# Performance work log

Measured on AMD Instinct MI355X. Metric: run time of the kernel, lower is better.

Reference implementation:

```python
import jax, jax.numpy as jnp
import numpy as np

ROUTINGS = 3
NUM_CAPSULE = 32
DIM_CAPSULE = 64
K_EPSILON = 1e-7  # keras K.epsilon()


def squash(x, axis=-1):
    s = jnp.sum(jnp.square(x), axis=axis, keepdims=True) + K_EPSILON
    scale = jnp.sqrt(s) / (0.5 + s)
    return scale * x


def setup_inputs() -> dict:
    key = jax.random.key(0)
    k1, k2 = jax.random.split(key)
    B, N_in, D_in = 32, 1024, 512
    u = jax.random.normal(k1, (B, N_in, D_in), dtype=jnp.float32)
    # glorot_uniform for capsule_kernel (conv1d width-1 kernel == dense matrix)
    fan_out = NUM_CAPSULE * DIM_CAPSULE
    limit = float(np.sqrt(6.0 / (D_in + fan_out)))
    W = jax.random.uniform(k2, (D_in, fan_out), jnp.float32, -limit, limit)
    return {"u": u, "W": W}


def reference(u, W):
    B, N_in, _ = u.shape
    # K.conv1d with width-1 kernel == matmul, then reshape
    u_hat = (u @ W).reshape(B, N_in, NUM_CAPSULE, DIM_CAPSULE)
    u_hat = jnp.transpose(u_hat, (0, 2, 1, 3))  # [B, N_out, N_in, D]
    b = jnp.zeros(u_hat.shape[:3], u_hat.dtype)  # [B, N_out, N_in]
    vj = None
    for i in range(ROUTINGS):
        Wv = jax.nn.softmax(b, axis=1)  # softmax over output capsules (axis=1)
        vj = jnp.einsum('bon,bond->bod', Wv, u_hat)  # batch_dot(Wv,u_hat,[2,2])
        if i < ROUTINGS - 1:
            # K.l2_normalize(vj) with default axis=None -> global L2 norm
            norm = jnp.sqrt(jnp.maximum(jnp.sum(jnp.square(vj)), 1e-12))
            vjn = vj / norm
            b = jnp.einsum('bod,bond->bon', vjn, u_hat)  # batch_dot(vj,u_hat,[2,3])
    return squash(vj)
```

## Files before the change

kernel.cpp:

```cpp
#include <hip/hip_runtime.h>
#include <hip/hip_bf16.h>


constexpr int B = 32, N = 1024, K = 512, O = 32, D = 64, F = 2048;
constexpr int NT = 32;
constexpr int ST = 72;
constexpr int STW = 40;

typedef __attribute__((ext_vector_type(8))) short bf16x8;
typedef __attribute__((ext_vector_type(4))) float f32x4;

__device__ inline unsigned int pk_hi(float x, float y) {
  union { __hip_bfloat162 h; unsigned int u; } c;
  c.h = __float22bfloat162_rn(float2{x, y});
  return c.u;
}
__device__ inline unsigned short bf16_1(float x) {
  return (unsigned short)(pk_hi(x, 0.f) & 0xffffu);
}
__device__ inline void split2(float x, unsigned short& h, unsigned short& l) {
  h = bf16_1(x);
  l = bf16_1(x - __uint_as_float((unsigned int)h << 16));
}
__device__ inline float bf2f(unsigned short h) {
  return __uint_as_float((unsigned int)h << 16);
}
__device__ inline int swz(int r) { return ((r >> 3) & 7) << 3; }

__device__ inline bf16x8 frag_row(const unsigned short* p, int r, int k0) {
  return *(const bf16x8*)&p[r * ST + (k0 ^ swz(r))];
}
__device__ inline bf16x8 frag_col(const unsigned short* p, int c, int n0) {
  bf16x8 f;
#pragma unroll
  for (int j = 0; j < 8; j++) {
    int n = n0 + j;
    f[j] = (short)p[n * ST + (c ^ swz(n))];
  }
  return f;
}

__global__ __launch_bounds__(256) void k_prep(const float* __restrict__ u,
                                              float* __restrict__ cs_part,
                                              unsigned short* __restrict__ u_bf) {
  __shared__ float4 red[128];
  int b = blockIdx.x, ntile = blockIdx.y, n0 = ntile * 32;
  int tid = threadIdx.x;
  int kq = (tid & 127) * 4, ng = tid >> 7;
  const float* ub = u + ((size_t)b * N + n0 + ng * 16) * K + kq;
  unsigned short* ubf = u_bf + ((size_t)b * N + n0 + ng * 16) * K + kq;
  float4 a = {0.f, 0.f, 0.f, 0.f};
#pragma unroll
  for (int nn = 0; nn < 16; nn++) {
    float4 v = *(const float4*)&ub[(size_t)nn * K];
    a.x += v.x; a.y += v.y; a.z += v.z; a.w += v.w;
    uint2 p;
    p.x = pk_hi(v.x, v.y);
    p.y = pk_hi(v.z, v.w);
    *(uint2*)&ubf[(size_t)nn * K] = p;
  }
  if (ng) red[tid & 127] = a;
  __syncthreads();
  if (!ng) {
    float4 o = red[tid];
    float* cs = cs_part + ((size_t)b * 32 + ntile) * K + kq;
    cs[0] = (a.x + o.x) * (1.f / 32.f);
    cs[1] = (a.y + o.y) * (1.f / 32.f);
    cs[2] = (a.z + o.z) * (1.f / 32.f);
    cs[3] = (a.w + o.w) * (1.f / 32.f);
  }
}

__global__ __launch_bounds__(512) void k_vjt(const unsigned short* __restrict__ Sp,
                                             const float* __restrict__ cs_part,
                                             const float* __restrict__ W,
                                             float* __restrict__ ssq_part, int slot,
                                             unsigned short* __restrict__ t_hi,
                                             unsigned short* __restrict__ t_lo) {
  __shared__ __align__(16) float s_s[K];
  __shared__ float red[7][D];
  __shared__ __align__(16) float vs[D];
  int bo = blockIdx.x, b = bo >> 5, o = bo & 31;
  int d = threadIdx.x & 63, ks = threadIdx.x >> 6;
  {
    int i = threadIdx.x;
    float a = 0.f;
    if (slot == 0) {
      const float* base = cs_part + (size_t)b * 32 * K;
#pragma unroll
      for (int nt = 0; nt < 32; nt++) a += base[(size_t)nt * K + i];
    } else {
      const unsigned short* base = Sp + ((size_t)b * NT * O + o) * K;
#pragma unroll
      for (int nt = 0; nt < NT; nt++) a += bf2f(base[(size_t)nt * O * K + i]);
    }
    s_s[i] = a;
  }
  __syncthreads();
  float acc = 0.f;
  const float* Wc = W + (size_t)o * D + d;
  for (int k = ks * 64; k < ks * 64 + 64; k += 4) {
    acc += s_s[k] * Wc[(size_t)k * F] + s_s[k + 1] * Wc[(size_t)(k + 1) * F] +
           s_s[k + 2] * Wc[(size_t)(k + 2) * F] + s_s[k + 3] * Wc[(size_t)(k + 3) * F];
  }
  if (ks) red[ks - 1][d] = acc;
  __syncthreads();
  if (ks == 0) {
#pragma unroll
    for (int j = 0; j < 7; j++) acc += red[j][d];
    vs[d] = acc;
    float ss = acc * acc;
#pragma unroll
    for (int m = 32; m >= 1; m >>= 1) ss += __shfl_xor(ss, m, 64);
    if (d == 0) ssq_part[slot * 1024 + bo] = ss;
  }
  __syncthreads();
  {
    int wave = threadIdx.x >> 6, lane = threadIdx.x & 63;
    int rr = lane >> 3, dc = lane & 7;
    float4 va = *(const float4*)&vs[dc * 8];
    float4 vb = *(const float4*)&vs[dc * 8 + 4];
#pragma unroll
    for (int i = 0; i < 8; i++) {
      int kk = wave * 64 + i * 8 + rr;
      const float* Wr = W + (size_t)kk * F + o * 64 + dc * 8;
      float4 wa = *(const float4*)Wr;
      float4 wb = *(const float4*)(Wr + 4);
      float p = wa.x * va.x + wa.y * va.y + wa.z * va.z + wa.w * va.w +
                wb.x * vb.x + wb.y * vb.y + wb.z * vb.z + wb.w * vb.w;
      p += __shfl_xor(p, 1, 64);
      p += __shfl_xor(p, 2, 64);
      p += __shfl_xor(p, 4, 64);
      if (dc == 0) {
        unsigned short h, l;
        split2(p, h, l);
        t_hi[(size_t)bo * K + kk] = h;
        t_lo[(size_t)bo * K + kk] = l;
      }
    }
  }
}

__global__ __launch_bounds__(512) void k_out(const unsigned short* __restrict__ Sp,
                                             const float* __restrict__ W,
                                             float* __restrict__ out) {
  __shared__ __align__(16) float s_s[K];
  __shared__ float red[7][D];
  int bo = blockIdx.x, b = bo >> 5, o = bo & 31;
  int d = threadIdx.x & 63, ks = threadIdx.x >> 6;
  {
    const unsigned short* base = Sp + ((size_t)b * NT * O + o) * K;
    int i = threadIdx.x;
    float a = 0.f;
#pragma unroll
    for (int nt = 0; nt < NT; nt++) a += bf2f(base[(size_t)nt * O * K + i]);
    s_s[i] = a;
  }
  __syncthreads();
  float acc = 0.f;
  const float* Wc = W + (size_t)o * D + d;
  for (int k = ks * 64; k < ks * 64 + 64; k += 4) {
    acc += s_s[k] * Wc[(size_t)k * F] + s_s[k + 1] * Wc[(size_t)(k + 1) * F] +
           s_s[k + 2] * Wc[(size_t)(k + 2) * F] + s_s[k + 3] * Wc[(size_t)(k + 3) * F];
  }
  if (ks) red[ks - 1][d] = acc;
  __syncthreads();
  if (ks == 0) {
#pragma unroll
    for (int j = 0; j < 7; j++) acc += red[j][d];
    float ss = acc * acc;
#pragma unroll
    for (int m = 32; m >= 1; m >>= 1) ss += __shfl_xor(ss, m, 64);
    float s = ss + 1e-7f;
    out[(size_t)bo * D + d] = (sqrtf(s) / (0.5f + s)) * acc;
  }
}

__global__ __launch_bounds__(256, 2) void k_route(const unsigned short* __restrict__ t_hi_g,
                                                  const unsigned short* __restrict__ t_lo_g,
                                                  const unsigned short* __restrict__ u_bf,
                                                  const float* __restrict__ ssq_part,
                                                  int slot,
                                                  unsigned short* __restrict__ Sp) {
  __shared__ unsigned short u_res[8][32 * ST];
  __shared__ float wv[32 * 36];
  __shared__ float psum[8 * 36];
  __shared__ float mbuf[36];
  __shared__ unsigned short wvh[32 * STW], wvl[32 * STW];

  const int b = blockIdx.x;
  const int tid = threadIdx.x, lane = tid & 63, wave = tid >> 6;
  const int m = lane & 15, oct = lane >> 4;
  const unsigned short* thg = t_hi_g + (size_t)b * O * K;
  const unsigned short* tlg = t_lo_g + (size_t)b * O * K;

  const int sr = tid >> 3, sc8 = (tid & 7) * 8;
  const int scs = sc8 ^ swz(sr);

  float nrm_inv;
  {
    const float* sp = ssq_part + slot * 1024;
    float sa = 0.f;
#pragma unroll
    for (int j = 0; j < 4; j++) sa += sp[tid + j * 256];
    psum[tid] = sa;
    __syncthreads();
    if (tid < 64) {
      float s = psum[tid] + psum[tid + 64] + psum[tid + 128] + psum[tid + 192];
#pragma unroll
      for (int mm = 32; mm >= 1; mm >>= 1) s += __shfl_xor(s, mm, 64);
      if (tid == 0) mbuf[0] = rsqrtf(fmaxf(s, 1e-12f));
    }
    __syncthreads();
    nrm_inv = mbuf[0];
  }

  const int mo = wave & 1, nt = wave >> 1;
  const int mo2 = wave & 1, kp = wave >> 1;
  const int o0 = mo2 * 16;

  for (int ti = 0; ti < 2; ti++) {
    const int tile = blockIdx.y * 2 + ti;
    const unsigned short* ubf = u_bf + ((size_t)b * N + tile * 32) * K;

    __syncthreads();
#pragma unroll
    for (int ch = 0; ch < 8; ch++) {
      *(uint4*)&u_res[ch][sr * ST + scs] =
          *(const uint4*)&ubf[(size_t)sr * K + ch * 64 + sc8];
    }
    __syncthreads();

    f32x4 accb = {0.f, 0.f, 0.f, 0.f};
    for (int kcb = 0; kcb < 8; kcb++) {
      const unsigned short* uc = u_res[kcb];
      const size_t tb = (size_t)(mo * 16 + m) * K + kcb * 64;
#pragma unroll
      for (int ks = 0; ks < 64; ks += 32) {
        bf16x8 ah = *(const bf16x8*)&thg[tb + ks + oct * 8];
        bf16x8 al = *(const bf16x8*)&tlg[tb + ks + oct * 8];
        bf16x8 bh = frag_row(uc, nt * 16 + m, ks + oct * 8);
        accb = __builtin_amdgcn_mfma_f32_16x16x32_bf16(ah, bh, accb, 0, 0, 0);
        accb = __builtin_amdgcn_mfma_f32_16x16x32_bf16(al, bh, accb, 0, 0, 0);
      }
    }
#pragma unroll
    for (int r = 0; r < 4; r++)
      wv[(mo * 16 + oct * 4 + r) * 36 + nt * 16 + m] = accb[r] * nrm_inv;
    __syncthreads();

    {
      int n = tid & 31, g = tid >> 5;
      float m4 = -1e30f;
#pragma unroll
      for (int j = 0; j < 4; j++) m4 = fmaxf(m4, wv[(g * 4 + j) * 36 + n]);
      psum[g * 36 + n] = m4;
      __syncthreads();
      if (tid < 32) {
        float mx = psum[tid];
#pragma unroll
        for (int gg = 1; gg < 8; gg++) mx = fmaxf(mx, psum[gg * 36 + tid]);
        mbuf[tid] = mx;
      }
      __syncthreads();
      float mx = mbuf[n];
      float s4 = 0.f;
#pragma unroll
      for (int j = 0; j < 4; j++) {
        float e = __expf(wv[(g * 4 + j) * 36 + n] - mx);
        wv[(g * 4 + j) * 36 + n] = e;
        s4 += e;
      }
      psum[g * 36 + n] = s4;
      __syncthreads();
      if (tid < 32) {
        float s = 0.f;
#pragma unroll
        for (int gg = 0; gg < 8; gg++) s += psum[gg * 36 + tid];
        mbuf[tid] = 1.f / s;
      }
      __syncthreads();
      float inv = mbuf[n];
#pragma unroll
      for (int j = 0; j < 4; j++) {
        unsigned short h, l;
        split2(wv[(g * 4 + j) * 36 + n] * inv, h, l);
        wvh[(g * 4 + j) * STW + n] = h;
        wvl[(g * 4 + j) * STW + n] = l;
      }
    }
    __syncthreads();

    bf16x8 a_h = *(const bf16x8*)&wvh[(o0 + m) * STW + oct * 8];
    bf16x8 a_l = *(const bf16x8*)&wvl[(o0 + m) * STW + oct * 8];
    unsigned short* Sb = Sp + ((size_t)b * NT + tile) * O * K;
    for (int kcb = 0; kcb < 8; kcb++) {
      const unsigned short* uc = u_res[kcb];
#pragma unroll
      for (int kt = kp * 2; kt < kp * 2 + 2; kt++) {
        int c = kt * 16 + m;
        bf16x8 bh = frag_col(uc, c, oct * 8);
        f32x4 acs = {0.f, 0.f, 0.f, 0.f};
        acs = __builtin_amdgcn_mfma_f32_16x16x32_bf16(a_h, bh, acs, 0, 0, 0);
        acs = __builtin_amdgcn_mfma_f32_16x16x32_bf16(a_l, bh, acs, 0, 0, 0);
#pragma unroll
        for (int r = 0; r < 4; r++)
          Sb[(size_t)(o0 + oct * 4 + r) * K + kcb * 64 + c] = bf16_1(acs[r]);
      }
    }
  }
}

extern "C" void kernel_launch(void* const* d_in, const int* in_sizes, int n_in,
                              void* d_out, int out_size, void* d_ws, size_t ws_size,
                              hipStream_t stream) {
  const float* u = (const float*)d_in[0];
  const float* W = (const float*)d_in[1];
  float* out = (float*)d_out;

  char* ws = (char*)d_ws;
  unsigned short* Sp = (unsigned short*)ws;
  unsigned short* u_bf = Sp + (size_t)B * NT * O * K;
  unsigned short* t_hi = u_bf + (size_t)B * N * K;
  unsigned short* t_lo = t_hi + (size_t)B * O * K;
  float* cs_part = (float*)(t_lo + (size_t)B * O * K);
  float* ssq_part = cs_part + (size_t)B * 32 * K;

  k_prep<<<dim3(B, 32), 256, 0, stream>>>(u, cs_part, u_bf);
  k_vjt<<<B * O, 512, 0, stream>>>(Sp, cs_part, W, ssq_part, 0, t_hi, t_lo);
  k_route<<<dim3(B, NT / 2), 256, 0, stream>>>(t_hi, t_lo, u_bf, ssq_part, 0, Sp);
  k_vjt<<<B * O, 512, 0, stream>>>(Sp, cs_part, W, ssq_part, 1, t_hi, t_lo);
  k_route<<<dim3(B, NT / 2), 256, 0, stream>>>(t_hi, t_lo, u_bf, ssq_part, 1, Sp);
  k_out<<<B * O, 512, 0, stream>>>(Sp, W, out);
}
```

Before: 189.1 us.

## Accumulate route partial sums across four tiles per block with register prefetch

k_route now handles four 32-row tiles per block, up from two, and keeps the weighted-sum partials in MFMA accumulator registers across those tiles. It writes one bf16 partial per slab instead of one per tile, which cuts the Sp partial buffer from 32 to 8 entries per (b,o) and reduces the reduction reads in k_vjt and k_out. The next tile of u is software-prefetched into registers while the current tile is being computed. The costs are higher register pressure (launch bounds relaxed to one block per SIMD group) and half as many route blocks (256), which may lower occupancy and latency hiding.

```diff
diff --git a/kernel.cpp b/kernel.cpp
--- a/kernel.cpp
+++ b/kernel.cpp
@@ -3,7 +3,7 @@
 
 
 constexpr int B = 32, N = 1024, K = 512, O = 32, D = 64, F = 2048;
-constexpr int NT = 32;
+constexpr int SLABS = 8;
 constexpr int ST = 72;
 constexpr int STW = 40;
 
@@ -90,9 +90,9 @@
 #pragma unroll
       for (int nt = 0; nt < 32; nt++) a += base[(size_t)nt * K + i];
     } else {
-      const unsigned short* base = Sp + ((size_t)b * NT * O + o) * K;
-#pragma unroll
-      for (int nt = 0; nt < NT; nt++) a += bf2f(base[(size_t)nt * O * K + i]);
+      const unsigned short* base = Sp + ((size_t)(b * O + o)) * (SLABS * K);
+#pragma unroll
+      for (int nt = 0; nt < SLABS; nt++) a += bf2f(base[nt * K + i]);
     }
     s_s[i] = a;
   }
@@ -149,11 +149,11 @@
   int bo = blockIdx.x, b = bo >> 5, o = bo & 31;
   int d = threadIdx.x & 63, ks = threadIdx.x >> 6;
   {
-    const unsigned short* base = Sp + ((size_t)b * NT * O + o) * K;
+    const unsigned short* base = Sp + ((size_t)(b * O + o)) * (SLABS * K);
     int i = threadIdx.x;
     float a = 0.f;
 #pragma unroll
-    for (int nt = 0; nt < NT; nt++) a += bf2f(base[(size_t)nt * O * K + i]);
+    for (int nt = 0; nt < SLABS; nt++) a += bf2f(base[nt * K + i]);
     s_s[i] = a;
   }
   __syncthreads();
@@ -176,7 +176,7 @@
   }
 }
 
-__global__ __launch_bounds__(256, 2) void k_route(const unsigned short* __restrict__ t_hi_g,
+__global__ __launch_bounds__(256, 1) void k_route(const unsigned short* __restrict__ t_hi_g,
                                                   const unsigned short* __restrict__ t_lo_g,
                                                   const unsigned short* __restrict__ u_bf,
                                                   const float* __restrict__ ssq_part,
@@ -188,7 +188,7 @@
   __shared__ float mbuf[36];
   __shared__ unsigned short wvh[32 * STW], wvl[32 * STW];
 
-  const int b = blockIdx.x;
+  const int b = blockIdx.x, slab = blockIdx.y;
   const int tid = threadIdx.x, lane = tid & 63, wave = tid >> 6;
   const int m = lane & 15, oct = lane >> 4;
   const unsigned short* thg = t_hi_g + (size_t)b * O * K;
@@ -197,6 +197,14 @@
   const int sr = tid >> 3, sc8 = (tid & 7) * 8;
   const int scs = sc8 ^ swz(sr);
 
+  uint4 pf[8];
+  {
+    const unsigned short* ub0 = u_bf + ((size_t)b * N + (slab * 4) * 32) * K;
+#pragma unroll
+    for (int ch = 0; ch < 8; ch++)
+      pf[ch] = *(const uint4*)&ub0[(size_t)sr * K + ch * 64 + sc8];
+  }
+
   float nrm_inv;
   {
     const float* sp = ssq_part + slot * 1024;
@@ -215,21 +223,30 @@
     nrm_inv = mbuf[0];
   }
 
-  const int mo = wave & 1, nt = wave >> 1;
+  const int mo = wave & 1, nt4 = wave >> 1;
   const int mo2 = wave & 1, kp = wave >> 1;
   const int o0 = mo2 * 16;
 
-  for (int ti = 0; ti < 2; ti++) {
-    const int tile = blockIdx.y * 2 + ti;
-    const unsigned short* ubf = u_bf + ((size_t)b * N + tile * 32) * K;
-
-    __syncthreads();
-#pragma unroll
-    for (int ch = 0; ch < 8; ch++) {
-      *(uint4*)&u_res[ch][sr * ST + scs] =
-          *(const uint4*)&ubf[(size_t)sr * K + ch * 64 + sc8];
-    }
-    __syncthreads();
+  f32x4 sacc[8][2];
+#pragma unroll
+  for (int i = 0; i < 8; i++) {
+    sacc[i][0] = f32x4{0.f, 0.f, 0.f, 0.f};
+    sacc[i][1] = f32x4{0.f, 0.f, 0.f, 0.f};
+  }
+
+  for (int ti = 0; ti < 4; ti++) {
+    __syncthreads();
+#pragma unroll
+    for (int ch = 0; ch < 8; ch++)
+      *(uint4*)&u_res[ch][sr * ST + scs] = pf[ch];
+    __syncthreads();
+    if (ti < 3) {
+      const unsigned short* ubn =
+          u_bf + ((size_t)b * N + (slab * 4 + ti + 1) * 32) * K;
+#pragma unroll
+      for (int ch = 0; ch < 8; ch++)
+        pf[ch] = *(const uint4*)&ubn[(size_t)sr * K + ch * 64 + sc8];
+    }
 
     f32x4 accb = {0.f, 0.f, 0.f, 0.f};
     for (int kcb = 0; kcb < 8; kcb++) {
@@ -239,14 +256,14 @@
       for (int ks = 0; ks < 64; ks += 32) {
         bf16x8 ah = *(const bf16x8*)&thg[tb + ks + oct * 8];
         bf16x8 al = *(const bf16x8*)&tlg[tb + ks + oct * 8];
-        bf16x8 bh = frag_row(uc, nt * 16 + m, ks + oct * 8);
+        bf16x8 bh = frag_row(uc, nt4 * 16 + m, ks + oct * 8);
         accb = __builtin_amdgcn_mfma_f32_16x16x32_bf16(ah, bh, accb, 0, 0, 0);
         accb = __builtin_amdgcn_mfma_f32_16x16x32_bf16(al, bh, accb, 0, 0, 0);
       }
     }
 #pragma unroll
     for (int r = 0; r < 4; r++)
-      wv[(mo * 16 + oct * 4 + r) * 36 + nt * 16 + m] = accb[r] * nrm_inv;
+      wv[(mo * 16 + oct * 4 + r) * 36 + nt4 * 16 + m] = accb[r] * nrm_inv;
     __syncthreads();
 
     {
@@ -291,21 +308,35 @@
     }
     __syncthreads();
 
-    bf16x8 a_h = *(const bf16x8*)&wvh[(o0 + m) * STW + oct * 8];
-    bf16x8 a_l = *(const bf16x8*)&wvl[(o0 + m) * STW + oct * 8];
-    unsigned short* Sb = Sp + ((size_t)b * NT + tile) * O * K;
-    for (int kcb = 0; kcb < 8; kcb++) {
-      const unsigned short* uc = u_res[kcb];
-#pragma unroll
-      for (int kt = kp * 2; kt < kp * 2 + 2; kt++) {
-        int c = kt * 16 + m;
-        bf16x8 bh = frag_col(uc, c, oct * 8);
-        f32x4 acs = {0.f, 0.f, 0.f, 0.f};
-        acs = __builtin_amdgcn_mfma_f32_16x16x32_bf16(a_h, bh, acs, 0, 0, 0);
-        acs = __builtin_amdgcn_mfma_f32_16x16x32_bf16(a_l, bh, acs, 0, 0, 0);
-#pragma unroll
-        for (int r = 0; r < 4; r++)
-          Sb[(size_t)(o0 + oct * 4 + r) * K + kcb * 64 + c] = bf16_1(acs[r]);
+    {
+      bf16x8 a_h = *(const bf16x8*)&wvh[(o0 + m) * STW + oct * 8];
+      bf16x8 a_l = *(const bf16x8*)&wvl[(o0 + m) * STW + oct * 8];
+#pragma unroll
+      for (int kcb = 0; kcb < 8; kcb++) {
+        const unsigned short* uc = u_res[kcb];
+#pragma unroll
+        for (int kti = 0; kti < 2; kti++) {
+          int c = (kp * 2 + kti) * 16 + m;
+          bf16x8 bh = frag_col(uc, c, oct * 8);
+          sacc[kcb][kti] =
+              __builtin_amdgcn_mfma_f32_16x16x32_bf16(a_h, bh, sacc[kcb][kti], 0, 0, 0);
+          sacc[kcb][kti] =
+              __builtin_amdgcn_mfma_f32_16x16x32_bf16(a_l, bh, sacc[kcb][kti], 0, 0, 0);
+        }
+      }
+    }
+  }
+
+#pragma unroll
+  for (int kcb = 0; kcb < 8; kcb++) {
+#pragma unroll
+    for (int kti = 0; kti < 2; kti++) {
+      int c = kcb * 64 + (kp * 2 + kti) * 16 + m;
+#pragma unroll
+      for (int r = 0; r < 4; r++) {
+        int orow = o0 + oct * 4 + r;
+        Sp[((size_t)(b * O + orow)) * (SLABS * K) + (size_t)slab * K + c] =
+            bf16_1(sacc[kcb][kti][r]);
       }
     }
   }
@@ -320,7 +351,7 @@
 
   char* ws = (char*)d_ws;
   unsigned short* Sp = (unsigned short*)ws;
-  unsigned short* u_bf = Sp + (size_t)B * NT * O * K;
+  unsigned short* u_bf = Sp + (size_t)B * O * SLABS * K;
   unsigned short* t_hi = u_bf + (size_t)B * N * K;
   unsigned short* t_lo = t_hi + (size_t)B * O * K;
   float* cs_part = (float*)(t_lo + (size_t)B * O * K);
@@ -328,8 +359,8 @@
 
   k_prep<<<dim3(B, 32), 256, 0, stream>>>(u, cs_part, u_bf);
   k_vjt<<<B * O, 512, 0, stream>>>(Sp, cs_part, W, ssq_part, 0, t_hi, t_lo);
-  k_route<<<dim3(B, NT / 2), 256, 0, stream>>>(t_hi, t_lo, u_bf, ssq_part, 0, Sp);
+  k_route<<<dim3(B, SLABS), 256, 0, stream>>>(t_hi, t_lo, u_bf, ssq_part, 0, Sp);
   k_vjt<<<B * O, 512, 0, stream>>>(Sp, cs_part, W, ssq_part, 1, t_hi, t_lo);
-  k_route<<<dim3(B, NT / 2), 256, 0, stream>>>(t_hi, t_lo, u_bf, ssq_part, 1, Sp);
+  k_route<<<dim3(B, SLABS), 256, 0, stream>>>(t_hi, t_lo, u_bf, ssq_part, 1, Sp);
   k_out<<<B * O, 512, 0, stream>>>(Sp, W, out);
 }
```

After: 211.7 us. 11.9% more time.

## Restructure routing kernel: one tile per block, unpadded swizzled LDS, register softmax

Applied to the files above, without the earlier changes.

k_route now processes a single 32-row tile per block instead of two and launches twice as many blocks. Its launch bound rises to 4 blocks per CU. The u tile is staged in LDS with stride 64 and an XOR swizzle instead of padded stride 72, which shrinks the shared footprint. The u tile load is issued before the norm reduction so the two can overlap. Softmax runs on register values with fewer barriers, dropping the wv staging buffer and mbuf. The aim is more occupancy, better latency hiding and fewer syncs, at the cost of possible LDS bank conflicts from the new swizzle on column reads.

```diff
diff --git a/kernel.cpp b/kernel.cpp
--- a/kernel.cpp
+++ b/kernel.cpp
@@ -4,7 +4,7 @@
 
 constexpr int B = 32, N = 1024, K = 512, O = 32, D = 64, F = 2048;
 constexpr int NT = 32;
-constexpr int ST = 72;
+constexpr int STU = 64;
 constexpr int STW = 40;
 
 typedef __attribute__((ext_vector_type(8))) short bf16x8;
@@ -25,17 +25,16 @@
 __device__ inline float bf2f(unsigned short h) {
   return __uint_as_float((unsigned int)h << 16);
 }
-__device__ inline int swz(int r) { return ((r >> 3) & 7) << 3; }
-
-__device__ inline bf16x8 frag_row(const unsigned short* p, int r, int k0) {
-  return *(const bf16x8*)&p[r * ST + (k0 ^ swz(r))];
-}
-__device__ inline bf16x8 frag_col(const unsigned short* p, int c, int n0) {
+
+__device__ inline bf16x8 frag_row_u(const unsigned short* p, int r, int k0) {
+  return *(const bf16x8*)&p[r * STU + (k0 ^ ((r & 7) << 3))];
+}
+__device__ inline bf16x8 frag_col_u(const unsigned short* p, int c, int n0) {
   bf16x8 f;
 #pragma unroll
   for (int j = 0; j < 8; j++) {
     int n = n0 + j;
-    f[j] = (short)p[n * ST + (c ^ swz(n))];
+    f[j] = (short)p[n * STU + (c ^ ((n & 7) << 3))];
   }
   return f;
 }
@@ -176,26 +175,31 @@
   }
 }
 
-__global__ __launch_bounds__(256, 2) void k_route(const unsigned short* __restrict__ t_hi_g,
+__global__ __launch_bounds__(256, 4) void k_route(const unsigned short* __restrict__ t_hi_g,
                                                   const unsigned short* __restrict__ t_lo_g,
                                                   const unsigned short* __restrict__ u_bf,
                                                   const float* __restrict__ ssq_part,
                                                   int slot,
                                                   unsigned short* __restrict__ Sp) {
-  __shared__ unsigned short u_res[8][32 * ST];
-  __shared__ float wv[32 * 36];
-  __shared__ float psum[8 * 36];
-  __shared__ float mbuf[36];
+  __shared__ unsigned short u_res[8][32 * STU];
   __shared__ unsigned short wvh[32 * STW], wvl[32 * STW];
-
-  const int b = blockIdx.x;
+  __shared__ float psum[256];
+  __shared__ float nb;
+
+  const int b = blockIdx.x, tile = blockIdx.y;
   const int tid = threadIdx.x, lane = tid & 63, wave = tid >> 6;
   const int m = lane & 15, oct = lane >> 4;
+  const unsigned short* ubf = u_bf + ((size_t)b * N + tile * 32) * K;
   const unsigned short* thg = t_hi_g + (size_t)b * O * K;
   const unsigned short* tlg = t_lo_g + (size_t)b * O * K;
 
   const int sr = tid >> 3, sc8 = (tid & 7) * 8;
-  const int scs = sc8 ^ swz(sr);
+  const int scs = sc8 ^ ((sr & 7) << 3);
+
+#pragma unroll
+  for (int ch = 0; ch < 8; ch++)
+    *(uint4*)&u_res[ch][sr * STU + scs] =
+        *(const uint4*)&ubf[(size_t)sr * K + ch * 64 + sc8];
 
   float nrm_inv;
   {
@@ -209,104 +213,78 @@
       float s = psum[tid] + psum[tid + 64] + psum[tid + 128] + psum[tid + 192];
 #pragma unroll
       for (int mm = 32; mm >= 1; mm >>= 1) s += __shfl_xor(s, mm, 64);
-      if (tid == 0) mbuf[0] = rsqrtf(fmaxf(s, 1e-12f));
-    }
-    __syncthreads();
-    nrm_inv = mbuf[0];
-  }
-
-  const int mo = wave & 1, nt = wave >> 1;
-  const int mo2 = wave & 1, kp = wave >> 1;
-  const int o0 = mo2 * 16;
-
-  for (int ti = 0; ti < 2; ti++) {
-    const int tile = blockIdx.y * 2 + ti;
-    const unsigned short* ubf = u_bf + ((size_t)b * N + tile * 32) * K;
-
-    __syncthreads();
-#pragma unroll
-    for (int ch = 0; ch < 8; ch++) {
-      *(uint4*)&u_res[ch][sr * ST + scs] =
-          *(const uint4*)&ubf[(size_t)sr * K + ch * 64 + sc8];
-    }
-    __syncthreads();
-
-    f32x4 accb = {0.f, 0.f, 0.f, 0.f};
-    for (int kcb = 0; kcb < 8; kcb++) {
-      const unsigned short* uc = u_res[kcb];
-      const size_t tb = (size_t)(mo * 16 + m) * K + kcb * 64;
-#pragma unroll
-      for (int ks = 0; ks < 64; ks += 32) {
-        bf16x8 ah = *(const bf16x8*)&thg[tb + ks + oct * 8];
-        bf16x8 al = *(const bf16x8*)&tlg[tb + ks + oct * 8];
-        bf16x8 bh = frag_row(uc, nt * 16 + m, ks + oct * 8);
-        accb = __builtin_amdgcn_mfma_f32_16x16x32_bf16(ah, bh, accb, 0, 0, 0);
-        accb = __builtin_amdgcn_mfma_f32_16x16x32_bf16(al, bh, accb, 0, 0, 0);
-      }
-    }
-#pragma unroll
-    for (int r = 0; r < 4; r++)
-      wv[(mo * 16 + oct * 4 + r) * 36 + nt * 16 + m] = accb[r] * nrm_inv;
-    __syncthreads();
-
-    {
-      int n = tid & 31, g = tid >> 5;
-      float m4 = -1e30f;
-#pragma unroll
-      for (int j = 0; j < 4; j++) m4 = fmaxf(m4, wv[(g * 4 + j) * 36 + n]);
-      psum[g * 36 + n] = m4;
-      __syncthreads();
-      if (tid < 32) {
-        float mx = psum[tid];
-#pragma unroll
-        for (int gg = 1; gg < 8; gg++) mx = fmaxf(mx, psum[gg * 36 + tid]);
-        mbuf[tid] = mx;
-      }
-      __syncthreads();
-      float mx = mbuf[n];
-      float s4 = 0.f;
-#pragma unroll
-      for (int j = 0; j < 4; j++) {
-        float e = __expf(wv[(g * 4 + j) * 36 + n] - mx);
-        wv[(g * 4 + j) * 36 + n] = e;
-        s4 += e;
-      }
-      psum[g * 36 + n] = s4;
-      __syncthreads();
-      if (tid < 32) {
-        float s = 0.f;
-#pragma unroll
-        for (int gg = 0; gg < 8; gg++) s += psum[gg * 36 + tid];
-        mbuf[tid] = 1.f / s;
-      }
-      __syncthreads();
-      float inv = mbuf[n];
-#pragma unroll
-      for (int j = 0; j < 4; j++) {
-        unsigned short h, l;
-        split2(wv[(g * 4 + j) * 36 + n] * inv, h, l);
-        wvh[(g * 4 + j) * STW + n] = h;
-        wvl[(g * 4 + j) * STW + n] = l;
-      }
-    }
-    __syncthreads();
-
-    bf16x8 a_h = *(const bf16x8*)&wvh[(o0 + m) * STW + oct * 8];
-    bf16x8 a_l = *(const bf16x8*)&wvl[(o0 + m) * STW + oct * 8];
-    unsigned short* Sb = Sp + ((size_t)b * NT + tile) * O * K;
-    for (int kcb = 0; kcb < 8; kcb++) {
-      const unsigned short* uc = u_res[kcb];
-#pragma unroll
-      for (int kt = kp * 2; kt < kp * 2 + 2; kt++) {
-        int c = kt * 16 + m;
-        bf16x8 bh = frag_col(uc, c, oct * 8);
-        f32x4 acs = {0.f, 0.f, 0.f, 0.f};
-        acs = __builtin_amdgcn_mfma_f32_16x16x32_bf16(a_h, bh, acs, 0, 0, 0);
-        acs = __builtin_amdgcn_mfma_f32_16x16x32_bf16(a_l, bh, acs, 0, 0, 0);
-#pragma unroll
-        for (int r = 0; r < 4; r++)
-          Sb[(size_t)(o0 + oct * 4 + r) * K + kcb * 64 + c] = bf16_1(acs[r]);
-      }
+      if (tid == 0) nb = rsqrtf(fmaxf(s, 1e-12f));
+    }
+    __syncthreads();
+    nrm_inv = nb;
+  }
+
+  const int mo = wave & 1, nt4 = wave >> 1;
+  f32x4 accb = {0.f, 0.f, 0.f, 0.f};
+  for (int kcb = 0; kcb < 8; kcb++) {
+    const unsigned short* uc = u_res[kcb];
+    const size_t tb = (size_t)(mo * 16 + m) * K + (size_t)kcb * 64;
+#pragma unroll
+    for (int ks = 0; ks < 64; ks += 32) {
+      bf16x8 ah = *(const bf16x8*)&thg[tb + ks + oct * 8];
+      bf16x8 al = *(const bf16x8*)&tlg[tb + ks + oct * 8];
+      bf16x8 bh = frag_row_u(uc, nt4 * 16 + m, ks + oct * 8);
+      accb = __builtin_amdgcn_mfma_f32_16x16x32_bf16(ah, bh, accb, 0, 0, 0);
+      accb = __builtin_amdgcn_mfma_f32_16x16x32_bf16(al, bh, accb, 0, 0, 0);
+    }
+  }
+
+  {
+    const int n = nt4 * 16 + m, g = mo * 4 + oct;
+    float v4[4];
+#pragma unroll
+    for (int r = 0; r < 4; r++) v4[r] = accb[r] * nrm_inv;
+    float m4 = fmaxf(fmaxf(v4[0], v4[1]), fmaxf(v4[2], v4[3]));
+    psum[g * 32 + n] = m4;
+    __syncthreads();
+    float mx = psum[n];
+#pragma unroll
+    for (int gg = 1; gg < 8; gg++) mx = fmaxf(mx, psum[gg * 32 + n]);
+    __syncthreads();
+    float e[4], s4 = 0.f;
+#pragma unroll
+    for (int r = 0; r < 4; r++) {
+      e[r] = __expf(v4[r] - mx);
+      s4 += e[r];
+    }
+    psum[g * 32 + n] = s4;
+    __syncthreads();
+    float s = 0.f;
+#pragma unroll
+    for (int gg = 0; gg < 8; gg++) s += psum[gg * 32 + n];
+    float inv = 1.f / s;
+#pragma unroll
+    for (int r = 0; r < 4; r++) {
+      unsigned short h, l;
+      split2(e[r] * inv, h, l);
+      wvh[(mo * 16 + oct * 4 + r) * STW + n] = h;
+      wvl[(mo * 16 + oct * 4 + r) * STW + n] = l;
+    }
+  }
+  __syncthreads();
+
+  const int kp = wave >> 1;
+  const int o0 = (wave & 1) * 16;
+  bf16x8 a_h = *(const bf16x8*)&wvh[(o0 + m) * STW + oct * 8];
+  bf16x8 a_l = *(const bf16x8*)&wvl[(o0 + m) * STW + oct * 8];
+  unsigned short* Sb = Sp + ((size_t)b * NT + tile) * O * K;
+  for (int kcb = 0; kcb < 8; kcb++) {
+    const unsigned short* uc = u_res[kcb];
+#pragma unroll
+    for (int kt = kp * 2; kt < kp * 2 + 2; kt++) {
+      int c = kt * 16 + m;
+      bf16x8 bh = frag_col_u(uc, c, oct * 8);
+      f32x4 acs = {0.f, 0.f, 0.f, 0.f};
+      acs = __builtin_amdgcn_mfma_f32_16x16x32_bf16(a_h, bh, acs, 0, 0, 0);
+      acs = __builtin_amdgcn_mfma_f32_16x16x32_bf16(a_l, bh, acs, 0, 0, 0);
+#pragma unroll
+      for (int r = 0; r < 4; r++)
+        Sb[(size_t)(o0 + oct * 4 + r) * K + kcb * 64 + c] = bf16_1(acs[r]);
     }
   }
 }
@@ -328,8 +306,8 @@
 
   k_prep<<<dim3(B, 32), 256, 0, stream>>>(u, cs_part, u_bf);
   k_vjt<<<B * O, 512, 0, stream>>>(Sp, cs_part, W, ssq_part, 0, t_hi, t_lo);
-  k_route<<<dim3(B, NT / 2), 256, 0, stream>>>(t_hi, t_lo, u_bf, ssq_part, 0, Sp);
+  k_route<<<dim3(B, NT), 256, 0, stream>>>(t_hi, t_lo, u_bf, ssq_part, 0, Sp);
   k_vjt<<<B * O, 512, 0, stream>>>(Sp, cs_part, W, ssq_part, 1, t_hi, t_lo);
-  k_route<<<dim3(B, NT / 2), 256, 0, stream>>>(t_hi, t_lo, u_bf, ssq_part, 1, Sp);
+  k_route<<<dim3(B, NT), 256, 0, stream>>>(t_hi, t_lo, u_bf, ssq_part, 1, Sp);
   k_out<<<B * O, 512, 0, stream>>>(Sp, W, out);
 }
```

Result: slower. 198.5 us (+5.0%).
